# Kernel tuning notes

Hardware: AMD Instinct MI355X
Metric: run time of the kernel (lower is better)

## Reference

```python
import jax, jax.numpy as jnp
import numpy as np

NUM_HEADS = 16
HEAD_DIM = 128
ROPE_BASE = 10000.0


def rotate_half(x):
    x1, x2 = jnp.split(x, 2, axis=-1)
    return jnp.concatenate((-x2, x1), axis=-1)


def rope_cos_sin(seq_len, dim, dtype):
    inv_freq = 1.0 / (ROPE_BASE ** (jnp.arange(0, dim, 2, dtype=jnp.float32) / dim))
    t = jnp.arange(seq_len, dtype=jnp.float32)
    freqs = jnp.einsum('i,j->ij', t, inv_freq)          # [S, dim/2]
    emb = jnp.concatenate((freqs, freqs), axis=-1)       # [S, dim]
    return emb.astype(dtype)  # caller applies cos/sin


def setup_inputs() -> dict:
    key = jax.random.key(0)
    k0, k1, k2, k3, k4 = jax.random.split(key, 5)
    B, S, H = 2, 2048, 2048
    hd = H // NUM_HEADS
    scale = 0.02
    return {
        'hidden_states': jax.random.normal(k0, (B, S, H), dtype=jnp.float32),
        'Wq': jax.random.normal(k1, (H, H), dtype=jnp.float32) * scale,
        'Wk': jax.random.normal(k2, (hd, H), dtype=jnp.float32) * scale,
        'Wv': jax.random.normal(k3, (hd, H), dtype=jnp.float32) * scale,
        'Wo': jax.random.normal(k4, (H, H), dtype=jnp.float32) * scale,
    }


def reference(hidden_states, Wq, Wk, Wv, Wo):
    B, S, H = hidden_states.shape
    nH, hd = NUM_HEADS, HEAD_DIM

    # projections (torch Linear: x @ W.T)
    q = jnp.einsum('bsh,oh->bso', hidden_states, Wq).reshape(B, S, nH, hd)
    q = q.transpose(0, 2, 1, 3)                          # [B, nH, S, hd]
    k = jnp.einsum('bsh,dh->bsd', hidden_states, Wk)      # [B, S, hd] single KV head
    v = jnp.einsum('bsh,dh->bsd', hidden_states, Wv)      # [B, S, hd]

    # rotary embedding
    emb = rope_cos_sin(S, hd, hidden_states.dtype)        # [S, hd]
    cos, sin = jnp.cos(emb), jnp.sin(emb)
    q = q * cos[None, None] + rotate_half(q) * sin[None, None]
    k = k * cos[None] + rotate_half(k) * sin[None]

    # attention: Q heads against shared K/V head
    scores = jnp.einsum('bhqd,bkd->bhqk', q, k) / jnp.sqrt(jnp.asarray(hd, hidden_states.dtype))
    attn = jax.nn.softmax(scores, axis=-1)               # dropout is identity in eval
    out = jnp.einsum('bhqk,bkd->bhqd', attn, v)           # [B, nH, S, hd]
    out = out.transpose(0, 2, 1, 3).reshape(B, S, H)
    attn_output = jnp.einsum('bsh,oh->bso', out, Wo)

    # cache tensors returned by the torch module: k, v with head dim of 1
    return attn_output, k[:, None], v[:, None]
```

## Files before the change

kernel.cpp:

```cpp
#include <hip/hip_runtime.h>
#include <hip/hip_bf16.h>

typedef __hip_bfloat16 bf16;

#define NH   16
#define HD   128
#define SEQ  2048
#define BB   2
#define HID  2048

#define ROPE_C 0.14391156856f

using frag   = __attribute__((ext_vector_type(8))) short;
using f32x4  = __attribute__((ext_vector_type(4))) float;
using f32x16 = __attribute__((ext_vector_type(16))) float;


__device__ __forceinline__ void cvt8_store(const float4 f0, const float4 f1, bf16* dst) {
    union { frag v; bf16 h[8]; } p;
    p.h[0] = __float2bfloat16(f0.x); p.h[1] = __float2bfloat16(f0.y);
    p.h[2] = __float2bfloat16(f0.z); p.h[3] = __float2bfloat16(f0.w);
    p.h[4] = __float2bfloat16(f1.x); p.h[5] = __float2bfloat16(f1.y);
    p.h[6] = __float2bfloat16(f1.z); p.h[7] = __float2bfloat16(f1.w);
    *reinterpret_cast<frag*>(dst) = p.v;
}

__device__ __forceinline__ unsigned pk2(float a, float b) {
    union { bf16 h[2]; unsigned u; } p;
    p.h[0] = __float2bfloat16(a);
    p.h[1] = __float2bfloat16(b);
    return p.u;
}

__device__ __forceinline__ void gld_lds16(const bf16* g, bf16* l) {
    __builtin_amdgcn_global_load_lds(
        (const __attribute__((address_space(1))) void*)g,
        (__attribute__((address_space(3))) void*)l, 16, 0, 0);
}

__global__ __launch_bounds__(256) void cvt_bf16(const float* __restrict__ hs,
                                                const float* __restrict__ Wq,
                                                const float* __restrict__ Wk,
                                                const float* __restrict__ Wv,
                                                bf16* __restrict__ hsb,
                                                bf16* __restrict__ wqb,
                                                bf16* __restrict__ wkb,
                                                bf16* __restrict__ wvb) {
    const int blk = blockIdx.x;
    const float* src;
    bf16* dst;
    if (blk < 4096)      { src = hs + (size_t)blk * 2048;          dst = hsb + (size_t)blk * 2048; }
    else if (blk < 6144) { src = Wq + (size_t)(blk - 4096) * 2048; dst = wqb + (size_t)(blk - 4096) * 2048; }
    else if (blk < 6272) { src = Wk + (size_t)(blk - 6144) * 2048; dst = wkb + (size_t)(blk - 6144) * 2048; }
    else                 { src = Wv + (size_t)(blk - 6272) * 2048; dst = wvb + (size_t)(blk - 6272) * 2048; }
    const int t = threadIdx.x * 8;
    const float4 f0 = *reinterpret_cast<const float4*>(src + t);
    const float4 f1 = *reinterpret_cast<const float4*>(src + t + 4);
    cvt8_store(f0, f1, dst + t);
}

__global__ __launch_bounds__(512) void gemm_qkv(const bf16* __restrict__ A,
                                                const bf16* __restrict__ Wqb,
                                                const bf16* __restrict__ Wkb,
                                                const bf16* __restrict__ Wvb,
                                                bf16* __restrict__ qout,
                                                float* __restrict__ Ck,
                                                float* __restrict__ Cv,
                                                bf16* __restrict__ kb,
                                                bf16* __restrict__ vt) {
    __shared__ bf16 Asl[4096];
    __shared__ bf16 Bsl[4096];
    const int tid  = threadIdx.x;
    const int wave = tid >> 6;
    const int lane = tid & 63;
    const int quad = lane >> 4;
    const int l15  = lane & 15;
    const int row0 = blockIdx.y * 128;
    const int bx   = blockIdx.x;
    const bool isq  = bx < 16;
    const bool is_v = (bx == 17);
    const bf16* W   = isq ? Wqb : (is_v ? Wvb : Wkb);
    const int col0  = isq ? bx * 128 : 0;

    const int sr = tid >> 2;
    const int sc = (tid & 3) * 8;

    const bf16* ag = A + (size_t)(row0 + sr) * HID + sc;
    const bf16* bg = W + (size_t)(col0 + sr) * HID + sc;
    bf16* al = &Asl[tid * 8];
    bf16* bl = &Bsl[tid * 8];

    f32x4 acc[8];
#pragma unroll
    for (int j = 0; j < 8; ++j) acc[j] = (f32x4){0.f,0.f,0.f,0.f};

    for (int k0 = 0; k0 < HID; k0 += 32) {
        __syncthreads();
        gld_lds16(ag + k0, al);
        gld_lds16(bg + k0, bl);
        __syncthreads();
        frag af, bfr[8];
        af = *reinterpret_cast<const frag*>(&Asl[(((wave*16 + l15)*4) + quad) * 8]);
#pragma unroll
        for (int j = 0; j < 8; ++j)
            bfr[j] = *reinterpret_cast<const frag*>(&Bsl[(((j*16 + l15)*4) + quad) * 8]);
#pragma unroll
        for (int j = 0; j < 8; ++j)
            acc[j] = __builtin_amdgcn_mfma_f32_16x16x32_bf16(af, bfr[j], acc[j], 0, 0, 0);
    }

    if (isq) {
#pragma unroll
        for (int r = 0; r < 4; ++r) {
            const int row = row0 + wave*16 + quad*4 + r;
            const int s = row & (SEQ - 1);
            bf16* crow = qout + (size_t)row * HID + col0;
#pragma unroll
            for (int j = 0; j < 4; ++j) {
                const int d = 16*j + l15;
                const float invf = expf(-(float)d * ROPE_C);
                float sn, cs;
                sincosf((float)s * invf, &sn, &cs);
                const float x1 = acc[j][r], x2 = acc[j+4][r];
                crow[d]      = __float2bfloat16(x1*cs - x2*sn);
                crow[d + 64] = __float2bfloat16(x2*cs + x1*sn);
            }
        }
    } else if (is_v) {
#pragma unroll
        for (int r = 0; r < 4; ++r) {
            const int row = row0 + wave*16 + quad*4 + r;
            const int s = row & (SEQ - 1);
            const int b = row >> 11;
            float* crow = Cv + (size_t)row * HD;
#pragma unroll
            for (int j = 0; j < 8; ++j) {
                const int d = 16*j + l15;
                const float val = acc[j][r];
                crow[d] = val;
                vt[((size_t)b * HD + d) * SEQ + s] = __float2bfloat16(val);
            }
        }
    } else {
#pragma unroll
        for (int r = 0; r < 4; ++r) {
            const int row = row0 + wave*16 + quad*4 + r;
            const int s = row & (SEQ - 1);
            float* crow = Ck + (size_t)row * HD;
#pragma unroll
            for (int j = 0; j < 4; ++j) {
                const int d = 16*j + l15;
                const float invf = expf(-(float)d * ROPE_C);
                float sn, cs;
                sincosf((float)s * invf, &sn, &cs);
                const float y1 = acc[j][r]*cs - acc[j+4][r]*sn;
                const float y2 = acc[j+4][r]*cs + acc[j][r]*sn;
                crow[d]      = y1;
                crow[d + 64] = y2;
                kb[(size_t)row * HD + d]      = __float2bfloat16(y1);
                kb[(size_t)row * HD + d + 64] = __float2bfloat16(y2);
            }
        }
    }
}

__global__ __launch_bounds__(256) void attn_mfma(const bf16* __restrict__ qbuf,
                                                 const bf16* __restrict__ kb,
                                                 const bf16* __restrict__ vt,
                                                 bf16* __restrict__ attn_out) {
    __shared__ char lds[32768];

    const int tid  = threadIdx.x;
    const int wave = tid >> 6;
    const int lane = tid & 63;
    const int l31  = lane & 31;
    const int h    = lane >> 5;
    const int qg   = wave & 1;
    const int kg   = wave >> 1;
    const int q0   = blockIdx.x * 64;
    const int hh   = blockIdx.y;
    const int b    = blockIdx.z;

    const bf16* kbb = kb + (size_t)b * SEQ * HD;
    const bf16* vtb = vt + (size_t)b * HD * SEQ;

    frag qfr[8];
    {
        const bf16* qrow = qbuf + ((size_t)(b * SEQ + q0 + qg * 32 + l31)) * HID + hh * HD;
#pragma unroll
        for (int c = 0; c < 8; ++c)
            qfr[c] = *reinterpret_cast<const frag*>(qrow + c * 16 + h * 8);
    }

    const int sl   = tid & 127;
    const int kg_s = tid >> 7;

    int klof[4];
#pragma unroll
    for (int i = 0; i < 4; ++i) {
        const int n   = sl + i * 128;
        const int key = n >> 4, d = (n >> 1) & 7, hs = n & 1;
        const int L   = d * 64 + key * 2 + hs;
        klof[i] = (kg_s * 8192 + L * 16) ^ (((((key >> 2) ^ d) & 7)) << 4);
    }
    int vlof[8], vgof[8];
#pragma unroll
    for (int i = 0; i < 8; ++i) {
        const int g   = sl + i * 128;
        const int dim = g >> 3, ks = (g >> 2) & 1, m = (g >> 1) & 1, hs = g & 1;
        const int dt  = dim >> 5;
        const int C   = (dt * 2 + ks) * 64 + (dim & 31) * 2 + hs;
        const int B   = 16384 + kg_s * 8192 + C * 16 + m * 8;
        const int xv  = (((dim & 31) >> 2) ^ (dt * 2 + ks)) & 7;
        vlof[i] = B ^ (xv << 4);
        vgof[i] = dim * SEQ + kg_s * 32 + (g & 7) * 4;
    }

    const int rpos = (l31 * 2 + h) * 16;
    const int rsw  = rpos ^ ((((rpos >> 7) & 7)) << 4);

    f32x16 oacc[4];
#pragma unroll
    for (int dt = 0; dt < 4; ++dt)
#pragma unroll
        for (int r = 0; r < 16; ++r) oacc[dt][r] = 0.f;
    float mrow = -1e30f;
    float lrow = 0.f;
    const float scale = 0.088388347648318433f;

    for (int it = 0; it < SEQ / 64; ++it) {
        __syncthreads();
        {
            const bf16* kp = kbb + (size_t)it * 64 * HD + kg_s * 4096;
            const bf16* vp = vtb + it * 64;
            uint4 krg[4];
            uint2 vrg[8];
#pragma unroll
            for (int i = 0; i < 4; ++i)
                krg[i] = *reinterpret_cast<const uint4*>(kp + (sl + i * 128) * 8);
#pragma unroll
            for (int i = 0; i < 8; ++i)
                vrg[i] = *reinterpret_cast<const uint2*>(vp + vgof[i]);
#pragma unroll
            for (int i = 0; i < 4; ++i)
                *reinterpret_cast<uint4*>(lds + klof[i]) = krg[i];
#pragma unroll
            for (int i = 0; i < 8; ++i)
                *reinterpret_cast<uint2*>(lds + vlof[i]) = vrg[i];
        }
        __syncthreads();

        f32x16 sacc;
#pragma unroll
        for (int r = 0; r < 16; ++r) sacc[r] = 0.f;
#pragma unroll
        for (int c = 0; c < 8; ++c) {
            const frag kf = *reinterpret_cast<const frag*>(
                lds + kg * 8192 + c * 1024 + (rsw ^ (c << 4)));
            sacc = __builtin_amdgcn_mfma_f32_32x32x16_bf16(kf, qfr[c], sacc, 0, 0, 0);
        }

        float mx = -1e30f;
#pragma unroll
        for (int r = 0; r < 16; ++r) mx = fmaxf(mx, sacc[r]);
        mx = fmaxf(mx, __shfl_xor(mx, 32));
        const bool skip = (bool)__all(mx - mrow <= 90.0f);
        const float mn = skip ? mrow : fmaxf(mrow, mx);
        const float al = skip ? 1.f : __expf((mrow - mn) * scale);
        float p[16];
        float ps = 0.f;
#pragma unroll
        for (int r = 0; r < 16; ++r) {
            p[r] = __expf((sacc[r] - mn) * scale);
            ps += p[r];
        }
        ps += __shfl_xor(ps, 32);
        lrow = lrow * al + ps;
        mrow = mn;

        frag pb[2];
#pragma unroll
        for (int ks = 0; ks < 2; ++ks) {
            union { unsigned u[4]; frag f; } pf;
#pragma unroll
            for (int w = 0; w < 4; ++w)
                pf.u[w] = pk2(p[8 * ks + 2 * w], p[8 * ks + 2 * w + 1]);
            pb[ks] = pf.f;
        }

        if (!skip)
#pragma unroll
            for (int dt = 0; dt < 4; ++dt)
#pragma unroll
                for (int r = 0; r < 16; ++r) oacc[dt][r] *= al;

#pragma unroll
        for (int dt = 0; dt < 4; ++dt)
#pragma unroll
            for (int ks = 0; ks < 2; ++ks) {
                const int cb = dt * 2 + ks;
                const frag vf = *reinterpret_cast<const frag*>(
                    lds + 16384 + kg * 8192 + cb * 1024 + (rsw ^ (cb << 4)));
                oacc[dt] = __builtin_amdgcn_mfma_f32_32x32x16_bf16(vf, pb[ks], oacc[dt], 0, 0, 0);
            }
    }

    __syncthreads();
    float* fl = reinterpret_cast<float*>(lds);
    if (h == 0) {
        fl[(qg * 2 + kg) * 32 + l31]       = mrow;
        fl[128 + (qg * 2 + kg) * 32 + l31] = lrow;
    }
    __syncthreads();
    const float m0 = fl[qg * 64 + l31],       m1 = fl[qg * 64 + 32 + l31];
    const float l0 = fl[128 + qg * 64 + l31], l1 = fl[128 + qg * 64 + 32 + l31];
    const float ms = fmaxf(m0, m1);
    const float c0 = __expf((m0 - ms) * scale);
    const float c1 = __expf((m1 - ms) * scale);
    const float inv = 1.f / (c0 * l0 + c1 * l1);
    const float cs = kg ? c1 : c0;
#pragma unroll
    for (int dt = 0; dt < 4; ++dt)
#pragma unroll
        for (int r = 0; r < 16; ++r) oacc[dt][r] *= cs;

    float* ob = reinterpret_cast<float*>(lds + 1024);
#pragma unroll
    for (int dt = 0; dt < 4; ++dt) {
        __syncthreads();
        if (kg == 1) {
            float* dst = ob + (qg * 64 + lane) * 17;
#pragma unroll
            for (int r = 0; r < 16; ++r) dst[r] = oacc[dt][r];
        }
        __syncthreads();
        if (kg == 0) {
            const float* sp = ob + (qg * 64 + lane) * 17;
            const int s = q0 + qg * 32 + l31;
            bf16* orow = attn_out + ((size_t)(b * SEQ + s)) * HID + hh * HD;
#pragma unroll
            for (int t = 0; t < 4; ++t) {
                const float v0 = (oacc[dt][t*4+0] + sp[t*4+0]) * inv;
                const float v1 = (oacc[dt][t*4+1] + sp[t*4+1]) * inv;
                const float v2 = (oacc[dt][t*4+2] + sp[t*4+2]) * inv;
                const float v3 = (oacc[dt][t*4+3] + sp[t*4+3]) * inv;
                uint2 val;
                val.x = pk2(v0, v1);
                val.y = pk2(v2, v3);
                *reinterpret_cast<uint2*>(orow + dt * 32 + t * 8 + h * 4) = val;
            }
        }
    }
}

__global__ __launch_bounds__(512) void gemm_o_mfma(const bf16* __restrict__ A,
                                                   const float* __restrict__ W,
                                                   float* __restrict__ C) {
    __shared__ bf16 Asl[4096];
    __shared__ bf16 Bsl[4096];
    const int tid  = threadIdx.x;
    const int wave = tid >> 6;
    const int lane = tid & 63;
    const int quad = lane >> 4;
    const int l15  = lane & 15;
    const int row0 = blockIdx.y * 128;
    const int col0 = blockIdx.x * 128;

    const int sr = tid >> 2;
    const int sc = (tid & 3) * 8;

    const bf16* ag = A + (size_t)(row0 + sr) * HID + sc;
    bf16* al = &Asl[tid * 8];

    f32x4 acc[8];
#pragma unroll
    for (int j = 0; j < 8; ++j) acc[j] = (f32x4){0.f,0.f,0.f,0.f};

    for (int k0 = 0; k0 < HID; k0 += 32) {
        __syncthreads();
        gld_lds16(ag + k0, al);
        {
            const float4* b0 = reinterpret_cast<const float4*>(W + (size_t)(col0 + sr) * HID + k0 + sc);
            cvt8_store(b0[0], b0[1], &Bsl[tid * 8]);
        }
        __syncthreads();
        frag af, bfr[8];
        af = *reinterpret_cast<const frag*>(&Asl[(((wave*16 + l15)*4) + quad) * 8]);
#pragma unroll
        for (int j = 0; j < 8; ++j)
            bfr[j] = *reinterpret_cast<const frag*>(&Bsl[(((j*16 + l15)*4) + quad) * 8]);
#pragma unroll
        for (int j = 0; j < 8; ++j)
            acc[j] = __builtin_amdgcn_mfma_f32_16x16x32_bf16(af, bfr[j], acc[j], 0, 0, 0);
    }

#pragma unroll
    for (int r = 0; r < 4; ++r) {
        const int row = row0 + wave*16 + quad*4 + r;
        float* crow = C + (size_t)row * HID + col0;
#pragma unroll
        for (int j = 0; j < 8; ++j)
            crow[16*j + l15] = acc[j][r];
    }
}

extern "C" void kernel_launch(void* const* d_in, const int* in_sizes, int n_in,
                              void* d_out, int out_size, void* d_ws, size_t ws_size,
                              hipStream_t stream) {
    const float* hs = (const float*)d_in[0];
    const float* Wq = (const float*)d_in[1];
    const float* Wk = (const float*)d_in[2];
    const float* Wv = (const float*)d_in[3];
    const float* Wo = (const float*)d_in[4];

    float* out      = (float*)d_out;
    float* out_attn = out;
    float* out_k    = out + 8388608;
    float* out_v    = out + 8388608 + 524288;

    bf16* qbuf = (bf16*)d_out;
    bf16* kb   = (bf16*)((char*)d_out + 16777216);
    bf16* vt   = (bf16*)((char*)d_out + 17825792);
    bf16* wqb  = (bf16*)((char*)d_out + 18874368);
    bf16* wkb  = (bf16*)((char*)d_out + 27262976);
    bf16* wvb  = (bf16*)((char*)d_out + 27787264);
    bf16* hsb      = (bf16*)d_ws;
    bf16* attn_out = (bf16*)d_ws;

    cvt_bf16  <<<dim3(6400),                  dim3(256), 0, stream>>>(hs, Wq, Wk, Wv, hsb, wqb, wkb, wvb);
    gemm_qkv  <<<dim3(18, (BB*SEQ)/128),      dim3(512), 0, stream>>>(hsb, wqb, wkb, wvb,
                                                                      qbuf, out_k, out_v, kb, vt);
    attn_mfma <<<dim3(SEQ/64, NH, BB),        dim3(256), 0, stream>>>(qbuf, kb, vt, attn_out);
    gemm_o_mfma<<<dim3(HID/128, (BB*SEQ)/128), dim3(512), 0, stream>>>(attn_out, Wo, out_attn);
}
```

Before: 377.7 us.

## Use 2x2 wave tiling with 64x64 per-wave tiles in QKV and O GEMMs

Both GEMM kernels move from 8 waves, each computing a 16x128 strip, to 4 waves arranged 2x2, each computing a 64x64 sub-tile with a 4x4 MFMA accumulator grid. Each wave now reuses every loaded A and B fragment across four MFMAs, which cuts LDS reads per MFMA. In the QKV kernel the B rows are permuted so that each wave holds matching RoPE halves (d and d+64), and the epilogue index mapping is adjusted to match. The cost is more accumulator registers per thread and half as many threads per block, with each thread now issuing twice the global-to-LDS loads.

```diff
diff --git a/kernel.cpp b/kernel.cpp
--- a/kernel.cpp
+++ b/kernel.cpp
@@ -59,15 +59,15 @@
     cvt8_store(f0, f1, dst + t);
 }
 
-__global__ __launch_bounds__(512) void gemm_qkv(const bf16* __restrict__ A,
-                                                const bf16* __restrict__ Wqb,
-                                                const bf16* __restrict__ Wkb,
-                                                const bf16* __restrict__ Wvb,
-                                                bf16* __restrict__ qout,
-                                                float* __restrict__ Ck,
-                                                float* __restrict__ Cv,
-                                                bf16* __restrict__ kb,
-                                                bf16* __restrict__ vt) {
+__global__ __launch_bounds__(256, 4) void gemm_qkv(const bf16* __restrict__ A,
+                                                   const bf16* __restrict__ Wqb,
+                                                   const bf16* __restrict__ Wkb,
+                                                   const bf16* __restrict__ Wvb,
+                                                   bf16* __restrict__ qout,
+                                                   float* __restrict__ Ck,
+                                                   float* __restrict__ Cv,
+                                                   bf16* __restrict__ kb,
+                                                   bf16* __restrict__ vt) {
     __shared__ bf16 Asl[4096];
     __shared__ bf16 Bsl[4096];
     const int tid  = threadIdx.x;
@@ -75,6 +75,8 @@
     const int lane = tid & 63;
     const int quad = lane >> 4;
     const int l15  = lane & 15;
+    const int wr   = wave >> 1;
+    const int wc   = wave & 1;
     const int row0 = blockIdx.y * 128;
     const int bx   = blockIdx.x;
     const bool isq  = bx < 16;
@@ -84,83 +86,98 @@
 
     const int sr = tid >> 2;
     const int sc = (tid & 3) * 8;
+    const int sg = ((sr >> 5) & 1) * 64 + (sr & 31);
 
     const bf16* ag = A + (size_t)(row0 + sr) * HID + sc;
-    const bf16* bg = W + (size_t)(col0 + sr) * HID + sc;
+    const bf16* bg = W + (size_t)(col0 + sg) * HID + sc;
     bf16* al = &Asl[tid * 8];
     bf16* bl = &Bsl[tid * 8];
 
-    f32x4 acc[8];
-#pragma unroll
-    for (int j = 0; j < 8; ++j) acc[j] = (f32x4){0.f,0.f,0.f,0.f};
+    f32x4 acc[4][4];
+#pragma unroll
+    for (int i = 0; i < 4; ++i)
+#pragma unroll
+        for (int j = 0; j < 4; ++j) acc[i][j] = (f32x4){0.f,0.f,0.f,0.f};
 
     for (int k0 = 0; k0 < HID; k0 += 32) {
         __syncthreads();
         gld_lds16(ag + k0, al);
+        gld_lds16(ag + (size_t)64 * HID + k0, al + 2048);
         gld_lds16(bg + k0, bl);
-        __syncthreads();
-        frag af, bfr[8];
-        af = *reinterpret_cast<const frag*>(&Asl[(((wave*16 + l15)*4) + quad) * 8]);
-#pragma unroll
-        for (int j = 0; j < 8; ++j)
-            bfr[j] = *reinterpret_cast<const frag*>(&Bsl[(((j*16 + l15)*4) + quad) * 8]);
-#pragma unroll
-        for (int j = 0; j < 8; ++j)
-            acc[j] = __builtin_amdgcn_mfma_f32_16x16x32_bf16(af, bfr[j], acc[j], 0, 0, 0);
+        gld_lds16(bg + (size_t)32 * HID + k0, bl + 2048);
+        __syncthreads();
+        frag af[4], bfr[4];
+#pragma unroll
+        for (int i = 0; i < 4; ++i)
+            af[i] = *reinterpret_cast<const frag*>(&Asl[(((wr*64 + i*16 + l15)*4) + quad) * 8]);
+#pragma unroll
+        for (int j = 0; j < 4; ++j)
+            bfr[j] = *reinterpret_cast<const frag*>(&Bsl[(((wc*64 + j*16 + l15)*4) + quad) * 8]);
+#pragma unroll
+        for (int i = 0; i < 4; ++i)
+#pragma unroll
+            for (int j = 0; j < 4; ++j)
+                acc[i][j] = __builtin_amdgcn_mfma_f32_16x16x32_bf16(af[i], bfr[j], acc[i][j], 0, 0, 0);
     }
 
     if (isq) {
 #pragma unroll
-        for (int r = 0; r < 4; ++r) {
-            const int row = row0 + wave*16 + quad*4 + r;
-            const int s = row & (SEQ - 1);
-            bf16* crow = qout + (size_t)row * HID + col0;
-#pragma unroll
-            for (int j = 0; j < 4; ++j) {
-                const int d = 16*j + l15;
-                const float invf = expf(-(float)d * ROPE_C);
-                float sn, cs;
-                sincosf((float)s * invf, &sn, &cs);
-                const float x1 = acc[j][r], x2 = acc[j+4][r];
-                crow[d]      = __float2bfloat16(x1*cs - x2*sn);
-                crow[d + 64] = __float2bfloat16(x2*cs + x1*sn);
+        for (int i = 0; i < 4; ++i)
+#pragma unroll
+            for (int r = 0; r < 4; ++r) {
+                const int row = row0 + wr*64 + i*16 + quad*4 + r;
+                const int s = row & (SEQ - 1);
+                bf16* crow = qout + (size_t)row * HID + col0;
+#pragma unroll
+                for (int j = 0; j < 2; ++j) {
+                    const int d = wc*32 + 16*j + l15;
+                    const float invf = expf(-(float)d * ROPE_C);
+                    float sn, cs;
+                    sincosf((float)s * invf, &sn, &cs);
+                    const float x1 = acc[i][j][r], x2 = acc[i][j+2][r];
+                    crow[d]      = __float2bfloat16(x1*cs - x2*sn);
+                    crow[d + 64] = __float2bfloat16(x2*cs + x1*sn);
+                }
             }
-        }
     } else if (is_v) {
 #pragma unroll
-        for (int r = 0; r < 4; ++r) {
-            const int row = row0 + wave*16 + quad*4 + r;
-            const int s = row & (SEQ - 1);
-            const int b = row >> 11;
-            float* crow = Cv + (size_t)row * HD;
-#pragma unroll
-            for (int j = 0; j < 8; ++j) {
-                const int d = 16*j + l15;
-                const float val = acc[j][r];
-                crow[d] = val;
-                vt[((size_t)b * HD + d) * SEQ + s] = __float2bfloat16(val);
+        for (int i = 0; i < 4; ++i)
+#pragma unroll
+            for (int r = 0; r < 4; ++r) {
+                const int row = row0 + wr*64 + i*16 + quad*4 + r;
+                const int s = row & (SEQ - 1);
+                const int b = row >> 11;
+                float* crow = Cv + (size_t)row * HD;
+#pragma unroll
+                for (int j = 0; j < 4; ++j) {
+                    const int d = (j >> 1)*64 + wc*32 + (j & 1)*16 + l15;
+                    const float val = acc[i][j][r];
+                    crow[d] = val;
+                    vt[((size_t)b * HD + d) * SEQ + s] = __float2bfloat16(val);
+                }
             }
-        }
     } else {
 #pragma unroll
-        for (int r = 0; r < 4; ++r) {
-            const int row = row0 + wave*16 + quad*4 + r;
-            const int s = row & (SEQ - 1);
-            float* crow = Ck + (size_t)row * HD;
-#pragma unroll
-            for (int j = 0; j < 4; ++j) {
-                const int d = 16*j + l15;
-                const float invf = expf(-(float)d * ROPE_C);
-                float sn, cs;
-                sincosf((float)s * invf, &sn, &cs);
-                const float y1 = acc[j][r]*cs - acc[j+4][r]*sn;
-                const float y2 = acc[j+4][r]*cs + acc[j][r]*sn;
-                crow[d]      = y1;
-                crow[d + 64] = y2;
-                kb[(size_t)row * HD + d]      = __float2bfloat16(y1);
-                kb[(size_t)row * HD + d + 64] = __float2bfloat16(y2);
+        for (int i = 0; i < 4; ++i)
+#pragma unroll
+            for (int r = 0; r < 4; ++r) {
+                const int row = row0 + wr*64 + i*16 + quad*4 + r;
+                const int s = row & (SEQ - 1);
+                float* crow = Ck + (size_t)row * HD;
+#pragma unroll
+                for (int j = 0; j < 2; ++j) {
+                    const int d = wc*32 + 16*j + l15;
+                    const float invf = expf(-(float)d * ROPE_C);
+                    float sn, cs;
+                    sincosf((float)s * invf, &sn, &cs);
+                    const float y1 = acc[i][j][r]*cs - acc[i][j+2][r]*sn;
+                    const float y2 = acc[i][j+2][r]*cs + acc[i][j][r]*sn;
+                    crow[d]      = y1;
+                    crow[d + 64] = y2;
+                    kb[(size_t)row * HD + d]      = __float2bfloat16(y1);
+                    kb[(size_t)row * HD + d + 64] = __float2bfloat16(y2);
+                }
             }
-        }
     }
 }
 
@@ -353,9 +370,9 @@
     }
 }
 
-__global__ __launch_bounds__(512) void gemm_o_mfma(const bf16* __restrict__ A,
-                                                   const float* __restrict__ W,
-                                                   float* __restrict__ C) {
+__global__ __launch_bounds__(256, 4) void gemm_o_mfma(const bf16* __restrict__ A,
+                                                      const float* __restrict__ W,
+                                                      float* __restrict__ C) {
     __shared__ bf16 Asl[4096];
     __shared__ bf16 Bsl[4096];
     const int tid  = threadIdx.x;
@@ -363,6 +380,8 @@
     const int lane = tid & 63;
     const int quad = lane >> 4;
     const int l15  = lane & 15;
+    const int wr   = wave >> 1;
+    const int wc   = wave & 1;
     const int row0 = blockIdx.y * 128;
     const int col0 = blockIdx.x * 128;
 
@@ -371,37 +390,50 @@
 
     const bf16* ag = A + (size_t)(row0 + sr) * HID + sc;
     bf16* al = &Asl[tid * 8];
-
-    f32x4 acc[8];
-#pragma unroll
-    for (int j = 0; j < 8; ++j) acc[j] = (f32x4){0.f,0.f,0.f,0.f};
+    const float* wg0 = W + (size_t)(col0 + sr) * HID + sc;
+    const float* wg1 = wg0 + (size_t)64 * HID;
+
+    f32x4 acc[4][4];
+#pragma unroll
+    for (int i = 0; i < 4; ++i)
+#pragma unroll
+        for (int j = 0; j < 4; ++j) acc[i][j] = (f32x4){0.f,0.f,0.f,0.f};
 
     for (int k0 = 0; k0 < HID; k0 += 32) {
         __syncthreads();
         gld_lds16(ag + k0, al);
+        gld_lds16(ag + (size_t)64 * HID + k0, al + 2048);
         {
-            const float4* b0 = reinterpret_cast<const float4*>(W + (size_t)(col0 + sr) * HID + k0 + sc);
+            const float4* b0 = reinterpret_cast<const float4*>(wg0 + k0);
+            const float4* b1 = reinterpret_cast<const float4*>(wg1 + k0);
             cvt8_store(b0[0], b0[1], &Bsl[tid * 8]);
-        }
-        __syncthreads();
-        frag af, bfr[8];
-        af = *reinterpret_cast<const frag*>(&Asl[(((wave*16 + l15)*4) + quad) * 8]);
-#pragma unroll
-        for (int j = 0; j < 8; ++j)
-            bfr[j] = *reinterpret_cast<const frag*>(&Bsl[(((j*16 + l15)*4) + quad) * 8]);
-#pragma unroll
-        for (int j = 0; j < 8; ++j)
-            acc[j] = __builtin_amdgcn_mfma_f32_16x16x32_bf16(af, bfr[j], acc[j], 0, 0, 0);
-    }
-
-#pragma unroll
-    for (int r = 0; r < 4; ++r) {
-        const int row = row0 + wave*16 + quad*4 + r;
-        float* crow = C + (size_t)row * HID + col0;
-#pragma unroll
-        for (int j = 0; j < 8; ++j)
-            crow[16*j + l15] = acc[j][r];
-    }
+            cvt8_store(b1[0], b1[1], &Bsl[tid * 8 + 2048]);
+        }
+        __syncthreads();
+        frag af[4], bfr[4];
+#pragma unroll
+        for (int i = 0; i < 4; ++i)
+            af[i] = *reinterpret_cast<const frag*>(&Asl[(((wr*64 + i*16 + l15)*4) + quad) * 8]);
+#pragma unroll
+        for (int j = 0; j < 4; ++j)
+            bfr[j] = *reinterpret_cast<const frag*>(&Bsl[(((wc*64 + j*16 + l15)*4) + quad) * 8]);
+#pragma unroll
+        for (int i = 0; i < 4; ++i)
+#pragma unroll
+            for (int j = 0; j < 4; ++j)
+                acc[i][j] = __builtin_amdgcn_mfma_f32_16x16x32_bf16(af[i], bfr[j], acc[i][j], 0, 0, 0);
+    }
+
+#pragma unroll
+    for (int i = 0; i < 4; ++i)
+#pragma unroll
+        for (int r = 0; r < 4; ++r) {
+            const int row = row0 + wr*64 + i*16 + quad*4 + r;
+            float* crow = C + (size_t)row * HID + col0 + wc*64;
+#pragma unroll
+            for (int j = 0; j < 4; ++j)
+                crow[16*j + l15] = acc[i][j][r];
+        }
 }
 
 extern "C" void kernel_launch(void* const* d_in, const int* in_sizes, int n_in,
@@ -428,8 +460,8 @@
     bf16* attn_out = (bf16*)d_ws;
 
     cvt_bf16  <<<dim3(6400),                  dim3(256), 0, stream>>>(hs, Wq, Wk, Wv, hsb, wqb, wkb, wvb);
-    gemm_qkv  <<<dim3(18, (BB*SEQ)/128),      dim3(512), 0, stream>>>(hsb, wqb, wkb, wvb,
+    gemm_qkv  <<<dim3(18, (BB*SEQ)/128),      dim3(256), 0, stream>>>(hsb, wqb, wkb, wvb,
                                                                       qbuf, out_k, out_v, kb, vt);
     attn_mfma <<<dim3(SEQ/64, NH, BB),        dim3(256), 0, stream>>>(qbuf, kb, vt, attn_out);
-    gemm_o_mfma<<<dim3(HID/128, (BB*SEQ)/128), dim3(512), 0, stream>>>(attn_out, Wo, out_attn);
-}
+    gemm_o_mfma<<<dim3(HID/128, (BB*SEQ)/128), dim3(256), 0, stream>>>(attn_out, Wo, out_attn);
+}
```

Measured after the change: 357.9 us. 5.2% less time.
